# Performance work log

Hardware: AMD Instinct MI355X
Metric: run time of the kernel (lower is better)

## Reference

```python
import jax, jax.numpy as jnp
import numpy as np

B = 32768
DIM = 768          # emb dim
NA = 1024          # outer n_anchors
K = 8              # n_comp (= n_patches P in relays)
PD = 16            # patch_dim
RD = K * PD        # relay_dim = 128
L = 2              # n_layers (relays)
RA = 16            # anchors per patch inside RelayLayer
NPH = 3            # n_phases
TD = NPH * RA      # tri_dim = 48
H = 64             # pw_hidden
MAG_MIN, MAG_MAX = 0.1, 5.0


def _nrm(x, eps=1e-12):
    return x / jnp.maximum(jnp.linalg.norm(x, axis=-1, keepdims=True), eps)


def _ln(x, g, b, eps=1e-5):
    mu = jnp.mean(x, axis=-1, keepdims=True)
    var = jnp.mean(jnp.square(x - mu), axis=-1, keepdims=True)
    return (x - mu) * jax.lax.rsqrt(var + eps) * g + b


def setup_inputs() -> dict:
    key = jax.random.key(0)
    ks = jax.random.split(key, 16)
    xav = lambda k, shp, fan_in, fan_out: jax.random.normal(k, shp, jnp.float32) * np.sqrt(2.0 / (fan_in + fan_out))
    home = _nrm(jax.random.normal(ks[3], (L, K, RA, PD), jnp.float32))
    anchors = _nrm(home + 0.05 * jax.random.normal(ks[4], (L, K, RA, PD), jnp.float32))
    return {
        'emb': jax.random.normal(ks[0], (B, DIM), jnp.float32),
        'triangulation': jax.random.normal(ks[1], (B, NA), jnp.float32),
        'raw_magnitude': jax.random.uniform(ks[2], (B, 1), jnp.float32),
        'emb_w': xav(ks[5], (DIM, RD // 2), DIM, RD // 2), 'emb_b': jnp.zeros((RD // 2,), jnp.float32),
        'tri_w': xav(ks[6], (NA, RD // 4), NA, RD // 4), 'tri_b': jnp.zeros((RD // 4,), jnp.float32),
        'ctx_w': xav(ks[7], (RD // 2 + RD // 4 + 1, RD), RD // 2 + RD // 4 + 1, RD), 'ctx_b': jnp.zeros((RD,), jnp.float32),
        'home': home, 'anchors': anchors,
        'pw_w1': xav(ks[8], (L, K, TD, H), TD, H), 'pw_b1': jnp.zeros((L, K, H), jnp.float32),
        'pw_w2': xav(ks[9], (L, K, H, PD), H, PD), 'pw_b2': jnp.zeros((L, K, PD), jnp.float32),
        'pwn_g': jnp.ones((L, PD), jnp.float32), 'pwn_b': jnp.zeros((L, PD), jnp.float32),
        'gates': jnp.full((L, K), -3.0, jnp.float32),
        'norm_g': jnp.ones((L, RD), jnp.float32), 'norm_b': jnp.zeros((L, RD), jnp.float32),
        'head_w1': xav(ks[10], (K, PD, PD // 2), PD, PD // 2), 'head_b1': jnp.zeros((K, PD // 2), jnp.float32),
        'head_w2': xav(ks[11], (K, PD // 2, 1), PD // 2, 1), 'head_b2': jnp.zeros((K, 1), jnp.float32),
        'stats_bias': jnp.zeros((K,), jnp.float32),
    }


def _relay(x, home, anchors, w1, b1, w2, b2, pg, pb, gates, ng, nb):
    Bb = x.shape[0]
    patches = _ln(x, ng, nb).reshape(Bb, K, PD)          # [B,P,d]
    pn = _nrm(patches)
    h = _nrm(home)                                       # [P,A,d]
    c = _nrm(anchors)
    cosw = jnp.clip(jnp.sum(h * c, axis=-1), -1 + 1e-7, 1 - 1e-7)
    omega = jnp.arccos(cosw)[..., None]                  # [P,A,1]
    so = jnp.maximum(jnp.sin(omega), 1e-7)
    tris = []
    for t in (0.0, 1.0 / 3.0, 2.0 / 3.0):
        at = _nrm((jnp.sin((1.0 - t) * omega) * h + jnp.sin(t * omega) * c) / so)
        tris.append(1.0 - jnp.einsum('bpd,pad->bpa', pn, at))
    tri = jnp.concatenate(tris, axis=-1)                 # [B,P,3A]
    hh = jax.nn.gelu(jnp.einsum('bpt,pth->bph', tri, w1) + b1, approximate=False)
    pw = _ln(jnp.einsum('bph,phd->bpd', hh, w2) + b2, pg, pb)
    g = jax.nn.sigmoid(gates)[None, :, None]             # [1,P,1]
    return x + (g * pw + (1.0 - g) * patches).reshape(Bb, -1)


def reference(emb, triangulation, raw_magnitude, emb_w, emb_b, tri_w, tri_b, ctx_w, ctx_b,
              home, anchors, pw_w1, pw_b1, pw_w2, pw_b2, pwn_g, pwn_b, gates, norm_g, norm_b,
              head_w1, head_b1, head_w2, head_b2, stats_bias):
    ctx = jnp.concatenate([emb @ emb_w + emb_b, triangulation @ tri_w + tri_b, raw_magnitude], axis=-1)
    x = ctx @ ctx_w + ctx_b                              # [B, RD]
    for l in range(L):
        x = _relay(x, home[l], anchors[l], pw_w1[l], pw_b1[l], pw_w2[l], pw_b2[l],
                   pwn_g[l], pwn_b[l], gates[l], norm_g[l], norm_b[l])
    patches = x.reshape(-1, K, PD)
    h1 = jax.nn.gelu(jnp.einsum('bkd,kdh->bkh', patches, head_w1) + head_b1, approximate=False)
    mc_raw = (jnp.einsum('bkh,kho->bko', h1, head_w2) + head_b2)[..., 0]   # [B,K]
    mc = MAG_MIN + (MAG_MAX - MAG_MIN) * jax.nn.sigmoid(mc_raw + stats_bias)
    mag = jnp.repeat(mc, NA // K, axis=-1)               # [B, NA]
    return (mag, mc)
```

## Files before the change

kernel.cpp:

```cpp
#include <hip/hip_runtime.h>
#include <hip/hip_bf16.h>
#include <math.h>

#define BTOT 32768

typedef float f32x4 __attribute__((ext_vector_type(4)));
typedef __bf16 v8bf __attribute__((ext_vector_type(8)));

__device__ float g_x[BTOT * 128];
__device__ float g_M[2 * 8 * 16 * 64];
__device__ float g_b1p[2 * 8 * 64];
__device__ __align__(16) unsigned short g_wf[1792 * 128];
__device__ float g_beff[128];
__device__ float g_wr[128];

__device__ __forceinline__ float fast_rcp(float x) {
#if __has_builtin(__builtin_amdgcn_rcpf)
    return __builtin_amdgcn_rcpf(x);
#else
    return 1.f / x;
#endif
}

__device__ __forceinline__ float gelu_f(float v) {
    const float p = v * fmaf(v * v, 0.0713548162f, 1.59576912f);
    return v * fast_rcp(1.f + __expf(-p));
}

__device__ __forceinline__ float fast_sigmoid(float v) {
    return fast_rcp(1.f + __expf(-v));
}

__device__ __forceinline__ unsigned short f2bf_rne(float x) {
    unsigned u = __float_as_uint(x);
    u += 0x7fffu + ((u >> 16) & 1u);
    return (unsigned short)(u >> 16);
}

#define GLOAD16(gp, lp)                                                        \
    __builtin_amdgcn_global_load_lds(                                          \
        (const __attribute__((address_space(1))) void*)(gp),                   \
        (__attribute__((address_space(3))) void*)(lp), 16, 0, 0)

__global__ __launch_bounds__(64) void k_pre(const float* __restrict__ home,
                                            const float* __restrict__ anchors,
                                            const float* __restrict__ pw_w1,
                                            const float* __restrict__ pw_b1) {
    __shared__ float s_AT[48 * 16];
    const int lp = blockIdx.x;
    const int tid = threadIdx.x;
    if (tid < 48) {
        const int t = tid >> 4, a = tid & 15;
        const float* hp = home + (lp * 16 + a) * 16;
        const float* cp = anchors + (lp * 16 + a) * 16;
        float h[16], c[16], nh = 0.f, nc = 0.f;
#pragma unroll
        for (int i = 0; i < 16; ++i) {
            h[i] = hp[i]; nh = fmaf(h[i], h[i], nh);
            c[i] = cp[i]; nc = fmaf(c[i], c[i], nc);
        }
        const float ih = 1.f / fmaxf(sqrtf(nh), 1e-12f);
        const float ic = 1.f / fmaxf(sqrtf(nc), 1e-12f);
        float cw = 0.f;
#pragma unroll
        for (int i = 0; i < 16; ++i) { h[i] *= ih; c[i] *= ic; cw = fmaf(h[i], c[i], cw); }
        cw = fminf(fmaxf(cw, -1.f + 1e-7f), 1.f - 1e-7f);
        const float om = acosf(cw);
        const float so = fmaxf(sinf(om), 1e-7f);
        const float tt = (float)t * (1.f / 3.f);
        const float s1 = sinf((1.f - tt) * om), s2 = sinf(tt * om);
        float v[16], nv = 0.f;
#pragma unroll
        for (int i = 0; i < 16; ++i) { v[i] = (s1 * h[i] + s2 * c[i]) / so; nv = fmaf(v[i], v[i], nv); }
        const float iv = 1.f / fmaxf(sqrtf(nv), 1e-12f);
#pragma unroll
        for (int i = 0; i < 16; ++i) s_AT[tid * 16 + i] = v[i] * iv;
    }
    __syncthreads();
    const int h = tid;
    const float* w1 = pw_w1 + lp * 48 * 64;
    float b = pw_b1[lp * 64 + h];
    float m[16];
#pragma unroll
    for (int d = 0; d < 16; ++d) m[d] = 0.f;
    for (int j = 0; j < 48; ++j) {
        const float w = w1[j * 64 + h];
        b += w;
#pragma unroll
        for (int d = 0; d < 16; ++d) m[d] = fmaf(s_AT[j * 16 + d], w, m[d]);
    }
    g_b1p[lp * 64 + h] = b;
#pragma unroll
    for (int d = 0; d < 16; ++d) g_M[(lp * 16 + d) * 64 + h] = m[d];
}

__global__ __launch_bounds__(256) void k_fold(const float* __restrict__ emb_w,
                                              const float* __restrict__ tri_w,
                                              const float* __restrict__ ctx_w,
                                              const float* __restrict__ ctx_b,
                                              const float* __restrict__ emb_b,
                                              const float* __restrict__ tri_b) {
    if (blockIdx.x == 56) {
        const int n = threadIdx.x;
        if (n < 128) {
            float b = ctx_b[n];
            for (int c = 0; c < 64; ++c) b = fmaf(emb_b[c], ctx_w[c * 128 + n], b);
            for (int c = 0; c < 32; ++c) b = fmaf(tri_b[c], ctx_w[(64 + c) * 128 + n], b);
            g_beff[n] = b;
            g_wr[n] = ctx_w[96 * 128 + n];
        }
        return;
    }
    __shared__ float sctx[97 * 128];
    for (int q = threadIdx.x; q < 3104; q += 256)
        *(float4*)&sctx[q * 4] = *(const float4*)&ctx_w[q * 4];
    __syncthreads();
    const int kt = blockIdx.x;
    const int kr = threadIdx.x >> 3;
    const int n0 = (threadIdx.x & 7) * 16;
    const int k = kt * 32 + kr;
    float acc[16];
#pragma unroll
    for (int j = 0; j < 16; ++j) acc[j] = 0.f;
    if (k < 768) {
        const float* wrow = emb_w + k * 64;
        for (int c = 0; c < 64; ++c) {
            const float a = wrow[c];
            const float* cx = &sctx[c * 128 + n0];
#pragma unroll
            for (int j = 0; j < 16; ++j) acc[j] = fmaf(a, cx[j], acc[j]);
        }
    } else {
        const float* wrow = tri_w + (k - 768) * 32;
        for (int c = 0; c < 32; ++c) {
            const float a = wrow[c];
            const float* cx = &sctx[(64 + c) * 128 + n0];
#pragma unroll
            for (int j = 0; j < 16; ++j) acc[j] = fmaf(a, cx[j], acc[j]);
        }
    }
    const int nt = threadIdx.x & 7;
    const int lanehi = (kr >> 3) << 4;
    const int j8 = kr & 7;
#pragma unroll
    for (int q = 0; q < 16; ++q) {
        const int lane = lanehi | q;
        g_wf[((kt * 8 + nt) * 64 + lane) * 8 + j8] = f2bf_rne(acc[q]);
    }
}

__global__ __launch_bounds__(128) void k_front_mfma(const float* __restrict__ emb,
                                                    const float* __restrict__ tri,
                                                    const float* __restrict__ rm) {
    __shared__ __align__(16) char lds[32768];
    const int tid = threadIdx.x;
    const int lane = tid & 63, w = tid >> 6;
    const int row0 = blockIdx.x * 32;
    const int arow = lane & 15, kgrp = lane >> 4;

    f32x4 acc[8];
#pragma unroll
    for (int nt = 0; nt < 8; ++nt) {
        f32x4 z = {0.f, 0.f, 0.f, 0.f};
        acc[nt] = z;
    }

    const float* embp = emb + (size_t)(row0 + w * 16 + arow) * 768 + kgrp * 8;
    const float* trip = tri + (size_t)(row0 + w * 16 + arow) * 1024 + kgrp * 8;

    float4 A0[4], A1[4];

#define ALOAD(kk, S) {                                                         \
        const float* ab_ = ((kk) < 12) ? (embp + (kk) * 64)                    \
                                       : (trip + ((kk) - 12) * 64);            \
        S[0] = *(const float4*)(ab_);                                          \
        S[1] = *(const float4*)(ab_ + 4);                                      \
        S[2] = *(const float4*)(ab_ + 32);                                     \
        S[3] = *(const float4*)(ab_ + 36);                                     \
    }

#define STAGE_B(kk, BUF) {                                                     \
        const char* gB_ = (const char*)g_wf + (size_t)(kk) * 16384             \
                          + w * 8192 + lane * 16;                              \
        char* Bb_ = lds + (BUF) * 16384 + w * 8192;               \
        _Pragma("unroll")                                                      \
        for (int i = 0; i < 8; ++i) GLOAD16(gB_ + i * 1024, Bb_ + i * 1024);   \
    }

#define COMPUTE(BUF, S) {                                                      \
        const char* Br_ = lds + (BUF) * 16384 + lane * 16;                     \
        _Pragma("unroll")                                                      \
        for (int h = 0; h < 2; ++h) {                                          \
            const float4 f0_ = S[h * 2], f1_ = S[h * 2 + 1];                   \
            v8bf a_;                                                           \
            a_[0] = (__bf16)f0_.x; a_[1] = (__bf16)f0_.y;                      \
            a_[2] = (__bf16)f0_.z; a_[3] = (__bf16)f0_.w;                      \
            a_[4] = (__bf16)f1_.x; a_[5] = (__bf16)f1_.y;                      \
            a_[6] = (__bf16)f1_.z; a_[7] = (__bf16)f1_.w;                      \
            const char* bp_ = Br_ + h * 8192;                                  \
            _Pragma("unroll")                                                  \
            for (int nt = 0; nt < 8; ++nt) {                                   \
                const v8bf b_ = *(const v8bf*)(bp_ + nt * 1024);               \
                acc[nt] = __builtin_amdgcn_mfma_f32_16x16x32_bf16(a_, b_, acc[nt], 0, 0, 0); \
            }                                                                  \
        }                                                                      \
    }

    ALOAD(0, A0);
    STAGE_B(0, 0);
    __syncthreads();
    for (int t = 0; t < 14; ++t) {
        ALOAD(2 * t + 1, A1);
        STAGE_B(2 * t + 1, 1);
        COMPUTE(0, A0);
        __syncthreads();
        if (t < 13) {
            ALOAD(2 * t + 2, A0);
            STAGE_B(2 * t + 2, 0);
        }
        COMPUTE(1, A1);
        __syncthreads();
    }
#undef ALOAD
#undef STAGE_B
#undef COMPUTE

    const int rowb = row0 + w * 16 + kgrp * 4;
    const f32x4 rv = *(const f32x4*)&rm[rowb];
#pragma unroll
    for (int nt = 0; nt < 8; ++nt) {
        const int col = nt * 16 + arow;
        const float be = g_beff[col];
        const float wv = g_wr[col];
#pragma unroll
        for (int rr = 0; rr < 4; ++rr) {
            g_x[(size_t)(rowb + rr) * 128 + col] = acc[nt][rr] + rv[rr] * wv + be;
        }
    }
}

__global__ __launch_bounds__(256) void k_relay(
    const float* __restrict__ pw_w2, const float* __restrict__ pw_b2,
    const float* __restrict__ pwn_g, const float* __restrict__ pwn_b,
    const float* __restrict__ gates, const float* __restrict__ norm_g,
    const float* __restrict__ norm_b, const float* __restrict__ head_w1,
    const float* __restrict__ head_b1, const float* __restrict__ head_w2,
    const float* __restrict__ head_b2, const float* __restrict__ stats_bias,
    float* __restrict__ out) {
    __shared__ __align__(16) float s_M[8 * 1028];
    __shared__ __align__(16) float s_w2[8 * 1028];
    __shared__ __align__(16) float s_b1p[8 * 68];
    __shared__ __align__(16) float s_hw1[8 * 132];
    __shared__ float s_hb1[64], s_hw2[64], s_hcb[8];
    __shared__ float s_mc[64 * 8];
    const int tid = threadIdx.x;
    const int pr = tid >> 3, p = tid & 7;
    const int rowA = blockIdx.x * 64 + pr * 2;

    {
        const int e = tid * 4, pp = e >> 7, rem = e & 127;
        *(float4*)&s_hw1[pp * 132 + rem] = *(const float4*)&head_w1[e];
    }
    if (tid < 64) { s_hb1[tid] = head_b1[tid]; s_hw2[tid] = head_w2[tid]; }
    if (tid < 8) s_hcb[tid] = head_b2[tid] + stats_bias[tid];

    float xA[16], xB[16];
    {
        const float* xp = g_x + (size_t)rowA * 128 + p * 16;
#pragma unroll
        for (int i = 0; i < 4; ++i) {
            *(float4*)&xA[i * 4] = *(const float4*)&xp[i * 4];
            *(float4*)&xB[i * 4] = *(const float4*)&xp[128 + i * 4];
        }
    }

    for (int l = 0; l < 2; ++l) {
        if (l) __syncthreads();
        for (int q = tid; q < 2048; q += 256) {
            const int e = q * 4, pp = e >> 10, rem = e & 1023;
            *(float4*)&s_M[pp * 1028 + rem] = *(const float4*)&g_M[l * 8192 + e];
            *(float4*)&s_w2[pp * 1028 + rem] = *(const float4*)&pw_w2[l * 8192 + e];
        }
        if (tid < 128) {
            const int e = tid * 4, pp = e >> 6, rem = e & 63;
            *(float4*)&s_b1p[pp * 68 + rem] = *(const float4*)&g_b1p[l * 512 + e];
        }
        __syncthreads();

        float sA = 0.f, qA = 0.f, sB = 0.f, qB = 0.f;
#pragma unroll
        for (int i = 0; i < 16; ++i) {
            sA += xA[i]; qA = fmaf(xA[i], xA[i], qA);
            sB += xB[i]; qB = fmaf(xB[i], xB[i], qB);
        }
#pragma unroll
        for (int m = 1; m < 8; m <<= 1) {
            sA += __shfl_xor(sA, m, 64); qA += __shfl_xor(qA, m, 64);
            sB += __shfl_xor(sB, m, 64); qB += __shfl_xor(qB, m, 64);
        }
        const float muA = sA * (1.f / 128.f);
        const float rsA = rsqrtf(fmaxf(qA * (1.f / 128.f) - muA * muA, 0.f) + 1e-5f);
        const float muB = sB * (1.f / 128.f);
        const float rsB = rsqrtf(fmaxf(qB * (1.f / 128.f) - muB * muB, 0.f) + 1e-5f);
        float paA[16], paB[16], nA = 0.f, nB = 0.f;
#pragma unroll
        for (int i = 0; i < 16; ++i) {
            const float gg = norm_g[l * 128 + p * 16 + i];
            const float bb = norm_b[l * 128 + p * 16 + i];
            const float vA = (xA[i] - muA) * rsA * gg + bb;
            const float vB = (xB[i] - muB) * rsB * gg + bb;
            paA[i] = vA; nA = fmaf(vA, vA, nA);
            paB[i] = vB; nB = fmaf(vB, vB, nB);
        }
        const float invA = 1.f / fmaxf(sqrtf(nA), 1e-12f);
        const float invB = 1.f / fmaxf(sqrtf(nB), 1e-12f);

        float pwA[16], pwB[16];
#pragma unroll
        for (int i = 0; i < 16; ++i) {
            const float b2 = pw_b2[(l * 8 + p) * 16 + i];
            pwA[i] = b2; pwB[i] = b2;
        }
        const float* Mp = &s_M[p * 1028];
        const float* W2p = &s_w2[p * 1028];
        const float* Bp = &s_b1p[p * 68];
        for (int h4 = 0; h4 < 16; ++h4) {
            float bq[4];
            *(float4*)bq = *(const float4*)&Bp[h4 * 4];
            float aA[4] = {0.f, 0.f, 0.f, 0.f};
            float aB[4] = {0.f, 0.f, 0.f, 0.f};
#pragma unroll
            for (int d = 0; d < 16; ++d) {
                float m4[4];
                *(float4*)m4 = *(const float4*)&Mp[d * 64 + h4 * 4];
#pragma unroll
                for (int j = 0; j < 4; ++j) {
                    aA[j] = fmaf(paA[d], m4[j], aA[j]);
                    aB[j] = fmaf(paB[d], m4[j], aB[j]);
                }
            }
#pragma unroll
            for (int j = 0; j < 4; ++j) {
                const float gA = gelu_f(bq[j] - invA * aA[j]);
                const float gB = gelu_f(bq[j] - invB * aB[j]);
                float w[16];
#pragma unroll
                for (int u = 0; u < 4; ++u)
                    *(float4*)&w[u * 4] = *(const float4*)&W2p[(h4 * 4 + j) * 16 + u * 4];
#pragma unroll
                for (int u = 0; u < 16; ++u) {
                    pwA[u] = fmaf(gA, w[u], pwA[u]);
                    pwB[u] = fmaf(gB, w[u], pwB[u]);
                }
            }
        }
        float s2A = 0.f, q2A = 0.f, s2B = 0.f, q2B = 0.f;
#pragma unroll
        for (int i = 0; i < 16; ++i) {
            s2A += pwA[i]; q2A = fmaf(pwA[i], pwA[i], q2A);
            s2B += pwB[i]; q2B = fmaf(pwB[i], pwB[i], q2B);
        }
        const float mu2A = s2A * (1.f / 16.f);
        const float rs2A = rsqrtf(fmaxf(q2A * (1.f / 16.f) - mu2A * mu2A, 0.f) + 1e-5f);
        const float mu2B = s2B * (1.f / 16.f);
        const float rs2B = rsqrtf(fmaxf(q2B * (1.f / 16.f) - mu2B * mu2B, 0.f) + 1e-5f);
        const float gate = fast_sigmoid(gates[l * 8 + p]);
#pragma unroll
        for (int i = 0; i < 16; ++i) {
            const float pg = pwn_g[l * 16 + i], pb = pwn_b[l * 16 + i];
            const float vA = (pwA[i] - mu2A) * rs2A * pg + pb;
            const float vB = (pwB[i] - mu2B) * rs2B * pg + pb;
            xA[i] = xA[i] + gate * vA + (1.f - gate) * paA[i];
            xB[i] = xB[i] + gate * vB + (1.f - gate) * paB[i];
        }
    }

    float accmA = s_hcb[p], accmB = accmA;
#pragma unroll
    for (int j = 0; j < 8; ++j) {
        float aA = s_hb1[p * 8 + j], aB = aA;
#pragma unroll
        for (int d = 0; d < 16; ++d) {
            const float w = s_hw1[p * 132 + d * 8 + j];
            aA = fmaf(xA[d], w, aA);
            aB = fmaf(xB[d], w, aB);
        }
        const float w2h = s_hw2[p * 8 + j];
        accmA = fmaf(gelu_f(aA), w2h, accmA);
        accmB = fmaf(gelu_f(aB), w2h, accmB);
    }
    const float mcA = 0.1f + 4.9f * fast_sigmoid(accmA);
    const float mcB = 0.1f + 4.9f * fast_sigmoid(accmB);
    s_mc[(pr * 2) * 8 + p] = mcA;
    s_mc[(pr * 2 + 1) * 8 + p] = mcB;
    out[(size_t)33554432 + (size_t)rowA * 8 + p] = mcA;
    out[(size_t)33554432 + (size_t)(rowA + 1) * 8 + p] = mcB;
    __syncthreads();

    const size_t base = (size_t)blockIdx.x * 64 * 1024;
#pragma unroll
    for (int it = 0; it < 64; ++it) {
        const int idx = it * 256 + tid;
        const int rr = idx >> 8, c4 = idx & 255;
        const float v = s_mc[rr * 8 + (c4 >> 5)];
        const float4 vv = make_float4(v, v, v, v);
        *(float4*)&out[base + rr * 1024 + c4 * 4] = vv;
    }
}

extern "C" void kernel_launch(void* const* d_in, const int* in_sizes, int n_in,
                              void* d_out, int out_size, void* d_ws, size_t ws_size,
                              hipStream_t stream) {
    (void)in_sizes; (void)n_in; (void)d_ws; (void)ws_size; (void)out_size;
    const float* emb = (const float*)d_in[0];
    const float* tria = (const float*)d_in[1];
    const float* rm = (const float*)d_in[2];
    const float* emb_w = (const float*)d_in[3];
    const float* emb_b = (const float*)d_in[4];
    const float* tri_w = (const float*)d_in[5];
    const float* tri_b = (const float*)d_in[6];
    const float* ctx_w = (const float*)d_in[7];
    const float* ctx_b = (const float*)d_in[8];
    const float* home = (const float*)d_in[9];
    const float* anch = (const float*)d_in[10];
    const float* pw_w1 = (const float*)d_in[11];
    const float* pw_b1 = (const float*)d_in[12];
    const float* pw_w2 = (const float*)d_in[13];
    const float* pw_b2 = (const float*)d_in[14];
    const float* pwn_g = (const float*)d_in[15];
    const float* pwn_b = (const float*)d_in[16];
    const float* gates = (const float*)d_in[17];
    const float* norm_g = (const float*)d_in[18];
    const float* norm_b = (const float*)d_in[19];
    const float* hw1 = (const float*)d_in[20];
    const float* hb1 = (const float*)d_in[21];
    const float* hw2 = (const float*)d_in[22];
    const float* hb2 = (const float*)d_in[23];
    const float* sb = (const float*)d_in[24];
    float* out = (float*)d_out;

    k_pre<<<16, 64, 0, stream>>>(home, anch, pw_w1, pw_b1);
    k_fold<<<57, 256, 0, stream>>>(emb_w, tri_w, ctx_w, ctx_b, emb_b, tri_b);
    k_front_mfma<<<1024, 128, 0, stream>>>(emb, tria, rm);
    k_relay<<<512, 256, 0, stream>>>(pw_w2, pw_b2, pwn_g, pwn_b, gates, norm_g, norm_b,
                                     hw1, hb1, hw2, hb2, sb, out);
}
```

Measured before the change: 174.6 us.

## Fuse MFMA front projection and relay kernels through shared memory

Merges the bf16 MFMA context-projection kernel and the relay/head kernel into one 256-thread kernel that handles 64 rows per block. The projected activations now stay in shared memory instead of being written to and read back from a global buffer, and one launch is removed. The B-staging work is split across four waves, and the shared-memory regions for the two stages are overlapped. The cost is a larger per-block LDS footprint (about 73 KB), which may lower occupancy for the bandwidth-heavy front GEMM.

```diff
diff --git a/kernel.cpp b/kernel.cpp
--- a/kernel.cpp
+++ b/kernel.cpp
@@ -7,7 +7,6 @@
 typedef float f32x4 __attribute__((ext_vector_type(4)));
 typedef __bf16 v8bf __attribute__((ext_vector_type(8)));
 
-__device__ float g_x[BTOT * 128];
 __device__ float g_M[2 * 8 * 16 * 64];
 __device__ float g_b1p[2 * 8 * 64];
 __device__ __align__(16) unsigned short g_wf[1792 * 128];
@@ -149,26 +148,45 @@
     }
 }
 
-__global__ __launch_bounds__(128) void k_front_mfma(const float* __restrict__ emb,
-                                                    const float* __restrict__ tri,
-                                                    const float* __restrict__ rm) {
-    __shared__ __align__(16) char lds[32768];
+__global__ __launch_bounds__(256) void k_fused(
+    const float* __restrict__ emb, const float* __restrict__ tri,
+    const float* __restrict__ rm,
+    const float* __restrict__ pw_w2, const float* __restrict__ pw_b2,
+    const float* __restrict__ pwn_g, const float* __restrict__ pwn_b,
+    const float* __restrict__ gates, const float* __restrict__ norm_g,
+    const float* __restrict__ norm_b, const float* __restrict__ head_w1,
+    const float* __restrict__ head_b1, const float* __restrict__ head_w2,
+    const float* __restrict__ head_b2, const float* __restrict__ stats_bias,
+    float* __restrict__ out) {
+    __shared__ __align__(16) char lds[74784];
+    float* const s_M   = (float*)lds;
+    float* const s_w2  = s_M + 8224;
+    float* const s_b1p = s_w2 + 8224;
+    float* const s_hw1 = s_b1p + 544;
+    float* const s_hb1 = s_hw1 + 1056;
+    float* const s_hw2 = s_hb1 + 64;
+    float* const s_hcb = s_hw2 + 64;
+    float* const s_mc  = s_hcb + 8;
+    float* const xs    = (float*)(lds + 32768);
+
     const int tid = threadIdx.x;
-    const int lane = tid & 63, w = tid >> 6;
-    const int row0 = blockIdx.x * 32;
-    const int arow = lane & 15, kgrp = lane >> 4;
-
-    f32x4 acc[8];
-#pragma unroll
-    for (int nt = 0; nt < 8; ++nt) {
-        f32x4 z = {0.f, 0.f, 0.f, 0.f};
-        acc[nt] = z;
-    }
-
-    const float* embp = emb + (size_t)(row0 + w * 16 + arow) * 768 + kgrp * 8;
-    const float* trip = tri + (size_t)(row0 + w * 16 + arow) * 1024 + kgrp * 8;
-
-    float4 A0[4], A1[4];
+    const int row0 = blockIdx.x * 64;
+
+    {
+        const int lane = tid & 63, w = tid >> 6;
+        const int arow = lane & 15, kgrp = lane >> 4;
+
+        f32x4 acc[8];
+#pragma unroll
+        for (int nt = 0; nt < 8; ++nt) {
+            f32x4 z = {0.f, 0.f, 0.f, 0.f};
+            acc[nt] = z;
+        }
+
+        const float* embp = emb + (size_t)(row0 + w * 16 + arow) * 768 + kgrp * 8;
+        const float* trip = tri + (size_t)(row0 + w * 16 + arow) * 1024 + kgrp * 8;
+
+        float4 A0[4], A1[4];
 
 #define ALOAD(kk, S) {                                                         \
         const float* ab_ = ((kk) < 12) ? (embp + (kk) * 64)                    \
@@ -181,10 +199,10 @@
 
 #define STAGE_B(kk, BUF) {                                                     \
         const char* gB_ = (const char*)g_wf + (size_t)(kk) * 16384             \
-                          + w * 8192 + lane * 16;                              \
-        char* Bb_ = lds + (BUF) * 16384 + w * 8192;               \
+                          + w * 4096 + lane * 16;                              \
+        char* Bb_ = lds + (BUF) * 16384 + w * 4096;               \
         _Pragma("unroll")                                                      \
-        for (int i = 0; i < 8; ++i) GLOAD16(gB_ + i * 1024, Bb_ + i * 1024);   \
+        for (int i = 0; i < 4; ++i) GLOAD16(gB_ + i * 1024, Bb_ + i * 1024);   \
     }
 
 #define COMPUTE(BUF, S) {                                                      \
@@ -206,73 +224,60 @@
         }                                                                      \
     }
 
-    ALOAD(0, A0);
-    STAGE_B(0, 0);
-    __syncthreads();
-    for (int t = 0; t < 14; ++t) {
-        ALOAD(2 * t + 1, A1);
-        STAGE_B(2 * t + 1, 1);
-        COMPUTE(0, A0);
+        ALOAD(0, A0);
+        STAGE_B(0, 0);
         __syncthreads();
-        if (t < 13) {
-            ALOAD(2 * t + 2, A0);
-            STAGE_B(2 * t + 2, 0);
-        }
-        COMPUTE(1, A1);
-        __syncthreads();
-    }
+        for (int t = 0; t < 14; ++t) {
+            ALOAD(2 * t + 1, A1);
+            STAGE_B(2 * t + 1, 1);
+            COMPUTE(0, A0);
+            __syncthreads();
+            if (t < 13) {
+                ALOAD(2 * t + 2, A0);
+                STAGE_B(2 * t + 2, 0);
+            }
+            COMPUTE(1, A1);
+            __syncthreads();
+        }
 #undef ALOAD
 #undef STAGE_B
 #undef COMPUTE
 
-    const int rowb = row0 + w * 16 + kgrp * 4;
-    const f32x4 rv = *(const f32x4*)&rm[rowb];
-#pragma unroll
-    for (int nt = 0; nt < 8; ++nt) {
-        const int col = nt * 16 + arow;
-        const float be = g_beff[col];
-        const float wv = g_wr[col];
-#pragma unroll
-        for (int rr = 0; rr < 4; ++rr) {
-            g_x[(size_t)(rowb + rr) * 128 + col] = acc[nt][rr] + rv[rr] * wv + be;
-        }
-    }
-}
-
-__global__ __launch_bounds__(256) void k_relay(
-    const float* __restrict__ pw_w2, const float* __restrict__ pw_b2,
-    const float* __restrict__ pwn_g, const float* __restrict__ pwn_b,
-    const float* __restrict__ gates, const float* __restrict__ norm_g,
-    const float* __restrict__ norm_b, const float* __restrict__ head_w1,
-    const float* __restrict__ head_b1, const float* __restrict__ head_w2,
-    const float* __restrict__ head_b2, const float* __restrict__ stats_bias,
-    float* __restrict__ out) {
-    __shared__ __align__(16) float s_M[8 * 1028];
-    __shared__ __align__(16) float s_w2[8 * 1028];
-    __shared__ __align__(16) float s_b1p[8 * 68];
-    __shared__ __align__(16) float s_hw1[8 * 132];
-    __shared__ float s_hb1[64], s_hw2[64], s_hcb[8];
-    __shared__ float s_mc[64 * 8];
-    const int tid = threadIdx.x;
+        const int lrow = w * 16 + kgrp * 4;
+        const f32x4 rv = *(const f32x4*)&rm[row0 + lrow];
+#pragma unroll
+        for (int nt = 0; nt < 8; ++nt) {
+            const int col = nt * 16 + arow;
+            const float be = g_beff[col];
+            const float wv = g_wr[col];
+#pragma unroll
+            for (int rr = 0; rr < 4; ++rr) {
+                xs[(lrow + rr) * 132 + col] = acc[nt][rr] + rv[rr] * wv + be;
+            }
+        }
+    }
+    __syncthreads();
+
     const int pr = tid >> 3, p = tid & 7;
-    const int rowA = blockIdx.x * 64 + pr * 2;
-
+    const int rowA = row0 + pr * 2;
+
+    float xA[16], xB[16];
+    {
+        const float* xpA = xs + (pr * 2) * 132 + p * 16;
+        const float* xpB = xs + (pr * 2 + 1) * 132 + p * 16;
+#pragma unroll
+        for (int i = 0; i < 4; ++i) {
+            *(float4*)&xA[i * 4] = *(const float4*)&xpA[i * 4];
+            *(float4*)&xB[i * 4] = *(const float4*)&xpB[i * 4];
+        }
+    }
     {
         const int e = tid * 4, pp = e >> 7, rem = e & 127;
         *(float4*)&s_hw1[pp * 132 + rem] = *(const float4*)&head_w1[e];
     }
     if (tid < 64) { s_hb1[tid] = head_b1[tid]; s_hw2[tid] = head_w2[tid]; }
     if (tid < 8) s_hcb[tid] = head_b2[tid] + stats_bias[tid];
-
-    float xA[16], xB[16];
-    {
-        const float* xp = g_x + (size_t)rowA * 128 + p * 16;
-#pragma unroll
-        for (int i = 0; i < 4; ++i) {
-            *(float4*)&xA[i * 4] = *(const float4*)&xp[i * 4];
-            *(float4*)&xB[i * 4] = *(const float4*)&xp[128 + i * 4];
-        }
-    }
+    __syncthreads();
 
     for (int l = 0; l < 2; ++l) {
         if (l) __syncthreads();
@@ -441,7 +446,7 @@
 
     k_pre<<<16, 64, 0, stream>>>(home, anch, pw_w1, pw_b1);
     k_fold<<<57, 256, 0, stream>>>(emb_w, tri_w, ctx_w, ctx_b, emb_b, tri_b);
-    k_front_mfma<<<1024, 128, 0, stream>>>(emb, tria, rm);
-    k_relay<<<512, 256, 0, stream>>>(pw_w2, pw_b2, pwn_g, pwn_b, gates, norm_g, norm_b,
-                                     hw1, hb1, hw2, hb2, sb, out);
-}
+    k_fused<<<512, 256, 0, stream>>>(emb, tria, rm, pw_w2, pw_b2, pwn_g, pwn_b,
+                                     gates, norm_g, norm_b, hw1, hb1, hw2, hb2,
+                                     sb, out);
+}
```

New measurement: 185.5 us. 6.2% more time.
